# Optimization experiments

Measured on AMD Instinct MI355X. Metric: run time of the kernel, lower is better.

## Reference

```python
import jax, jax.numpy as jnp
import numpy as np
import math

NEG_INF = -1000000000.0
D_EMBED = 1024
D_K = 1024
N_HEADS = 16
D_H = D_EMBED // N_HEADS


def setup_inputs() -> dict:
    key = jax.random.key(0)
    ks = jax.random.split(key, 12)
    B, S = 2, 2048
    s = 0.02
    return {
        "embed": jax.random.normal(ks[0], (B, S, D_EMBED), dtype=jnp.float32),
        "key": jax.random.normal(ks[1], (B, S, D_K), dtype=jnp.float32),
        "attn_mask": jax.random.randint(ks[2], (B, S, S), 0, 2, dtype=jnp.int32),
        "Wq": jax.random.normal(ks[3], (D_EMBED, D_EMBED), dtype=jnp.float32) * s,
        "bq": jnp.zeros((D_EMBED,), dtype=jnp.float32),
        "Wk": jax.random.normal(ks[4], (D_EMBED, D_K), dtype=jnp.float32) * s,
        "bk": jnp.zeros((D_EMBED,), dtype=jnp.float32),
        "Wv": jax.random.normal(ks[5], (D_EMBED, D_K), dtype=jnp.float32) * s,
        "bv": jnp.zeros((D_EMBED,), dtype=jnp.float32),
        "Wo": jax.random.normal(ks[6], (D_EMBED, D_EMBED), dtype=jnp.float32) * s,
        "bo": jnp.zeros((D_EMBED,), dtype=jnp.float32),
    }


def _alibi_bias(seq_len: int, n_heads: int) -> jnp.ndarray:
    # symmetric |i-j| distances, slopes 2^-(8k/H) for k=1..H
    r = jnp.arange(seq_len)
    pos = jnp.abs(r[None, :] - r[:, None]).astype(jnp.float32)  # [S, S]
    step = 8.0 / n_heads
    ms = 2.0 ** (-jnp.arange(step, 8.0 + step, step, dtype=jnp.float32))  # [H]
    return ms[:, None, None] * pos[None, :, :]  # [H, S, S]


def reference(embed, key, attn_mask, Wq, bq, Wk, bk, Wv, bv, Wo, bo):
    B, Sq, _ = embed.shape
    Sk = key.shape[1]
    Q = embed @ Wq.T + bq          # [B, Sq, D]
    K = key @ Wk.T + bk            # [B, Sk, D]
    V = key @ Wv.T + bv            # [B, Sk, D]
    Qh = Q.reshape(B, Sq, N_HEADS, D_H).transpose(0, 2, 1, 3)  # [B, H, Sq, d_h]
    Kh = K.reshape(B, Sk, N_HEADS, D_H).transpose(0, 2, 1, 3)
    Vh = V.reshape(B, Sk, N_HEADS, D_H).transpose(0, 2, 1, 3)
    attn = jnp.einsum("bhqd,bhkd->bhqk", Qh, Kh)
    # ALiBi bias subtracted BEFORE scaling (as in source)
    attn = attn - _alibi_bias(Sq, N_HEADS)[None]
    attn = attn * (1.0 / math.sqrt(D_EMBED))  # note: scale uses d_embed, not d_h
    attn = jnp.where(attn_mask[:, None, :, :] == 0, NEG_INF, attn)
    attn = jax.nn.softmax(attn, axis=-1)
    out = jnp.einsum("bhqk,bhkd->bhqd", attn, Vh)
    out = out.transpose(0, 2, 1, 3).reshape(B, Sq, D_EMBED)
    return out @ Wo.T + bo
```

## Files before the change

kernel.cpp:

```cpp
#include <hip/hip_runtime.h>


typedef _Float16 f16;
typedef __attribute__((ext_vector_type(8))) _Float16 f16x8;
typedef __attribute__((ext_vector_type(4))) _Float16 f16x4;
typedef __attribute__((ext_vector_type(4))) float f32x4;
typedef unsigned long long u64;
typedef unsigned int u32;

#define MFMA16 __builtin_amdgcn_mfma_f32_16x16x32_f16

__global__ __launch_bounds__(256) void k_convert(
    const float* __restrict__ embed, const float* __restrict__ key,
    const float* __restrict__ wq, const float* __restrict__ wk,
    const float* __restrict__ wv, const float* __restrict__ wo,
    f16* __restrict__ xe, f16* __restrict__ xk,
    f16* __restrict__ wqh, f16* __restrict__ wkh,
    f16* __restrict__ wvh, f16* __restrict__ woh)
{
    long g = (long)blockIdx.x * 256 + threadIdx.x;
    const float* src; f16* dst; long off;
    if (g < 524288)       { src = embed; dst = xe; off = g; }
    else if (g < 1048576) { src = key;   dst = xk; off = g - 524288; }
    else {
        long t = g - 1048576; int wi = (int)(t >> 17); off = t & 131071;
        if (wi == 0)      { src = wq; dst = wqh; }
        else if (wi == 1) { src = wk; dst = wkh; }
        else if (wi == 2) { src = wv; dst = wvh; }
        else              { src = wo; dst = woh; }
    }
    const float4* s4 = (const float4*)src;
    float4 a = s4[off * 2], b = s4[off * 2 + 1];
    f16x8 o;
    o[0]=(f16)a.x; o[1]=(f16)a.y; o[2]=(f16)a.z; o[3]=(f16)a.w;
    o[4]=(f16)b.x; o[5]=(f16)b.y; o[6]=(f16)b.z; o[7]=(f16)b.w;
    *(f16x8*)(dst + off * 8) = o;
}

__global__ __launch_bounds__(256) void k_packmask(
    const int* __restrict__ mask, u64* __restrict__ bits)
{
    int gw = (blockIdx.x * 256 + threadIdx.x) >> 6;
    int lane = threadIdx.x & 63;
    const int* row = mask + (long)gw * 2048;
    u64* out = bits + (long)gw * 32;
    #pragma unroll 4
    for (int c = 0; c < 32; ++c) {
        int v = row[c * 64 + lane];
        u64 b = __ballot(v != 0);
        if (lane == 0) out[c] = b;
    }
}

__global__ __launch_bounds__(256) void k_qkv(
    const f16* __restrict__ xe, const f16* __restrict__ xk,
    const f16* __restrict__ wqh, const f16* __restrict__ wkh, const f16* __restrict__ wvh,
    const float* __restrict__ bq, const float* __restrict__ bk, const float* __restrict__ bv,
    f16* __restrict__ Qh, f16* __restrict__ Kh, f16* __restrict__ Vt)
{
    int bid = blockIdx.x;
    int which = bid >> 8;
    int rr_ = bid & 255;
    int tm = rr_ >> 3, tn = rr_ & 7;
    const f16* X = (which == 0) ? xe : xk;
    const f16* W = (which == 0) ? wqh : (which == 1) ? wkh : wvh;
    const float* bias = (which == 0) ? bq : (which == 1) ? bk : bv;

    __shared__ f16 smem[128 * 136];
    f16* la = smem;
    f16* lb = smem + 128 * 64;

    int tid = threadIdx.x;
    int lane = tid & 63, wid = tid >> 6;
    int wr = wid >> 1, wc = wid & 1;
    int lm = lane & 15, qd = lane >> 4;

    f32x4 acc[4][4];
    #pragma unroll
    for (int i = 0; i < 4; i++)
        #pragma unroll
        for (int j = 0; j < 4; j++) acc[i][j] = (f32x4)0.0f;

    int m0 = tm * 128, n0 = tn * 128;

    for (int kt = 0; kt < 16; ++kt) {
        int k0 = kt * 64;
        __syncthreads();
        #pragma unroll
        for (int t = 0; t < 4; ++t) {
            int cid = tid + t * 256;
            int row = cid >> 3;
            int cg = cid & 7;
            int sw = cg ^ (row & 7);
            *(f16x8*)&la[row * 64 + sw * 8] =
                *(const f16x8*)&X[(long)(m0 + row) * 1024 + k0 + cg * 8];
            *(f16x8*)&lb[row * 64 + sw * 8] =
                *(const f16x8*)&W[(long)(n0 + row) * 1024 + k0 + cg * 8];
        }
        __syncthreads();
        #pragma unroll
        for (int ks = 0; ks < 2; ++ks) {
            f16x8 af[4], bfr[4];
            #pragma unroll
            for (int i = 0; i < 4; i++) {
                int m = 64 * wr + 16 * i + lm;
                int g = (ks * 4 + qd) ^ (m & 7);
                af[i] = *(const f16x8*)&la[m * 64 + g * 8];
                int n = 64 * wc + 16 * i + lm;
                int g2 = (ks * 4 + qd) ^ (n & 7);
                bfr[i] = *(const f16x8*)&lb[n * 64 + g2 * 8];
            }
            #pragma unroll
            for (int i = 0; i < 4; i++)
                #pragma unroll
                for (int j = 0; j < 4; j++)
                    acc[i][j] = MFMA16(af[i], bfr[j], acc[i][j], 0, 0, 0);
        }
    }

    if (which == 2) {
        #pragma unroll
        for (int j = 0; j < 4; j++) {
            int n = n0 + 64 * wc + 16 * j + lm;
            float bb = bias[n];
            int h = n >> 6, d = n & 63;
            #pragma unroll
            for (int i = 0; i < 4; i++) {
                int mbase = m0 + 64 * wr + 16 * i + 4 * qd;
                f16x4 pk;
                #pragma unroll
                for (int r = 0; r < 4; ++r) pk[r] = (f16)(acc[i][j][r] + bb);
                int b = mbase >> 11, s = mbase & 2047;
                *(f16x4*)&Vt[(((long)(b * 16 + h)) * 64 + d) * 2048 + s] = pk;
            }
        }
    } else {
        f16* dst = (which == 0) ? Qh : Kh;
        __syncthreads();
        #pragma unroll
        for (int j = 0; j < 4; j++) {
            int col = 64 * wc + 16 * j + lm;
            float bb = bias[n0 + col];
            #pragma unroll
            for (int i = 0; i < 4; i++) {
                int row = 64 * wr + 16 * i + 4 * qd;
                #pragma unroll
                for (int r = 0; r < 4; ++r)
                    smem[(row + r) * 136 + col] = (f16)(acc[i][j][r] + bb);
            }
        }
        __syncthreads();
        #pragma unroll
        for (int t = 0; t < 8; ++t) {
            int ci = tid + t * 256;
            int row = ci >> 4, cg = ci & 15;
            f16x8 v = *(const f16x8*)&smem[row * 136 + cg * 8];
            int m = m0 + row;
            int b = m >> 11, s = m & 2047;
            int h = (n0 >> 6) + (cg >> 3);
            int d0 = (cg & 7) * 8;
            *(f16x8*)&dst[(((long)(b * 16 + h)) * 2048 + s) * 64 + d0] = v;
        }
    }
}

__global__ __launch_bounds__(512, 4) void k_attn(
    const f16* __restrict__ Qh, const f16* __restrict__ Kh, const f16* __restrict__ Vt,
    const u64* __restrict__ mbits, f16* __restrict__ O)
{
    int bid = blockIdx.x;
    int qt = bid & 15;
    int h = (bid >> 4) & 15;
    int b = bid >> 8;
    int q0 = qt * 128;

    const f16* Qg = Qh + ((long)(b * 16 + h)) * 2048 * 64;
    const f16* Kg = Kh + ((long)(b * 16 + h)) * 2048 * 64;
    const f16* Vg = Vt + ((long)(b * 16 + h)) * 64 * 2048;

    __shared__ f16 ks[128 * 64];
    __shared__ f16 vs[64 * 128];
    __shared__ f16 ps[8][16 * 128];

    int tid = threadIdx.x, lane = tid & 63, wid = tid >> 6;
    int lm = lane & 15, qd = lane >> 4;

    int qrow = q0 + 16 * wid + lm;
    const u64* Mrow = mbits + ((long)(b * 2048) + qrow) * 32;

    f16x8 aq[2];
    #pragma unroll
    for (int ksi = 0; ksi < 2; ++ksi)
        aq[ksi] = *(const f16x8*)&Qg[(long)qrow * 64 + ksi * 32 + qd * 8];

    f32x4 oacc[4], lacc;
    #pragma unroll
    for (int c = 0; c < 4; c++) oacc[c] = (f32x4)0.0f;
    lacc = (f32x4)0.0f;
    f16x8 vone;
    #pragma unroll
    for (int j = 0; j < 8; j++) vone[j] = (f16)1.0f;

    const float c1 = 0.0450842252f;
    float negc2 = -__builtin_amdgcn_exp2f(-0.5f * (float)(h + 1)) * c1;
    const float c3 = 5.7707801634f;

    for (int kt = 0; kt < 16; ++kt) {
        int k0 = kt * 128;
        __syncthreads();
        #pragma unroll
        for (int t = 0; t < 2; ++t) {
            int cid = tid + t * 512;
            int row = cid >> 3, cg = cid & 7;
            int sw = cg ^ (row & 7);
            *(f16x8*)&ks[row * 64 + sw * 8] =
                *(const f16x8*)&Kg[(long)(k0 + row) * 64 + cg * 8];
            int vrow = cid >> 4, vg = cid & 15;
            int vsw = vg ^ (vrow & 7);
            *(f16x8*)&vs[vrow * 128 + vsw * 8] =
                *(const f16x8*)&Vg[(long)vrow * 2048 + k0 + vg * 8];
        }
        __syncthreads();

        u64 w0 = Mrow[kt * 2], w1 = Mrow[kt * 2 + 1];

        f32x4 sacc[8];
        #pragma unroll
        for (int c = 0; c < 8; c++) sacc[c] = (f32x4)0.0f;
        #pragma unroll
        for (int ksi = 0; ksi < 2; ++ksi) {
            #pragma unroll
            for (int c = 0; c < 8; c++) {
                int kr = 16 * c + lm;
                int g = (ksi * 4 + qd) ^ (kr & 7);
                f16x8 ak = *(const f16x8*)&ks[kr * 64 + g * 8];
                sacc[c] = MFMA16(ak, aq[ksi], sacc[c], 0, 0, 0);
            }
        }

        float qmkb = (float)(qrow - k0 - 4 * qd);
        int shb = 4 * qd;
        #pragma unroll
        for (int c = 0; c < 8; c++) {
            u32 nib = (u32)(((c < 4) ? w0 : w1) >> (16 * (c & 3) + shb)) & 15u;
            float qmkc = qmkb - 16.0f * (float)c;
            float p[4];
            #pragma unroll
            for (int r = 0; r < 4; ++r) {
                float t2 = fmaf(sacc[c][r], c1, -c3);
                float dd = qmkc - (float)r;
                float u = fmaf(fabsf(dd), negc2, t2);
                u = ((nib >> r) & 1u) ? u : -1e30f;
                p[r] = __builtin_amdgcn_exp2f(u);
            }
            f16x4 pk;
            #pragma unroll
            for (int r = 0; r < 4; ++r) pk[r] = (f16)p[r];
            int g8 = (2 * c + (qd >> 1)) ^ (lm & 7);
            *(f16x4*)&ps[wid][lm * 128 + g8 * 8 + (qd & 1) * 4] = pk;
        }

        #pragma unroll
        for (int k4 = 0; k4 < 4; ++k4) {
            int gp = (k4 * 4 + qd) ^ (lm & 7);
            f16x8 pa = *(const f16x8*)&ps[wid][lm * 128 + gp * 8];
            #pragma unroll
            for (int cc = 0; cc < 4; ++cc) {
                int d = 16 * cc + lm;
                int g = (k4 * 4 + qd) ^ (d & 7);
                f16x8 vb = *(const f16x8*)&vs[d * 128 + g * 8];
                oacc[cc] = MFMA16(pa, vb, oacc[cc], 0, 0, 0);
            }
            lacc = MFMA16(pa, vone, lacc, 0, 0, 0);
        }
    }

    #pragma unroll
    for (int r = 0; r < 4; ++r) {
        float linv = 1.0f / fmaxf(lacc[r], 1e-30f);
        long rowbase = ((long)(b * 2048 + q0 + 16 * wid + 4 * qd + r)) * 1024 + h * 64;
        #pragma unroll
        for (int cc = 0; cc < 4; ++cc)
            O[rowbase + 16 * cc + lm] = (f16)(oacc[cc][r] * linv);
    }
}

__global__ __launch_bounds__(256) void k_proj(
    const f16* __restrict__ Oh, const f16* __restrict__ woh,
    const float* __restrict__ bo, float* __restrict__ out)
{
    int bid = blockIdx.x;
    int tm = bid >> 3, tn = bid & 7;

    __shared__ f16 la[128 * 64];
    __shared__ f16 lb[128 * 64];

    int tid = threadIdx.x;
    int lane = tid & 63, wid = tid >> 6;
    int wr = wid >> 1, wc = wid & 1;
    int lm = lane & 15, qd = lane >> 4;

    f32x4 acc[4][4];
    #pragma unroll
    for (int i = 0; i < 4; i++)
        #pragma unroll
        for (int j = 0; j < 4; j++) acc[i][j] = (f32x4)0.0f;

    int m0 = tm * 128, n0 = tn * 128;

    for (int kt = 0; kt < 16; ++kt) {
        int k0 = kt * 64;
        __syncthreads();
        #pragma unroll
        for (int t = 0; t < 4; ++t) {
            int cid = tid + t * 256;
            int row = cid >> 3;
            int cg = cid & 7;
            int sw = cg ^ (row & 7);
            *(f16x8*)&la[row * 64 + sw * 8] =
                *(const f16x8*)&Oh[(long)(m0 + row) * 1024 + k0 + cg * 8];
            *(f16x8*)&lb[row * 64 + sw * 8] =
                *(const f16x8*)&woh[(long)(n0 + row) * 1024 + k0 + cg * 8];
        }
        __syncthreads();
        #pragma unroll
        for (int ks = 0; ks < 2; ++ks) {
            f16x8 af[4], bfr[4];
            #pragma unroll
            for (int i = 0; i < 4; i++) {
                int m = 64 * wr + 16 * i + lm;
                int g = (ks * 4 + qd) ^ (m & 7);
                af[i] = *(const f16x8*)&la[m * 64 + g * 8];
                int n = 64 * wc + 16 * i + lm;
                int g2 = (ks * 4 + qd) ^ (n & 7);
                bfr[i] = *(const f16x8*)&lb[n * 64 + g2 * 8];
            }
            #pragma unroll
            for (int i = 0; i < 4; i++)
                #pragma unroll
                for (int j = 0; j < 4; j++)
                    acc[i][j] = MFMA16(af[i], bfr[j], acc[i][j], 0, 0, 0);
        }
    }

    #pragma unroll
    for (int j = 0; j < 4; j++) {
        int n = n0 + 64 * wc + 16 * j + lm;
        float bb = bo[n];
        #pragma unroll
        for (int i = 0; i < 4; i++) {
            int mbase = m0 + 64 * wr + 16 * i + 4 * qd;
            #pragma unroll
            for (int r = 0; r < 4; ++r)
                out[(long)(mbase + r) * 1024 + n] = acc[i][j][r] + bb;
        }
    }
}

extern "C" void kernel_launch(void* const* d_in, const int* in_sizes, int n_in,
                              void* d_out, int out_size, void* d_ws, size_t ws_size,
                              hipStream_t stream)
{
    const float* embed = (const float*)d_in[0];
    const float* key   = (const float*)d_in[1];
    const int*   mask  = (const int*)d_in[2];
    const float* Wq = (const float*)d_in[3];
    const float* bq = (const float*)d_in[4];
    const float* Wk = (const float*)d_in[5];
    const float* bk = (const float*)d_in[6];
    const float* Wv = (const float*)d_in[7];
    const float* bv = (const float*)d_in[8];
    const float* Wo = (const float*)d_in[9];
    const float* bo = (const float*)d_in[10];

    char* ws = (char*)d_ws;
    f16* xe  = (f16*)(ws + 0);
    f16* xk  = (f16*)(ws + 8388608);
    f16* wqh = (f16*)(ws + 16777216);
    f16* wkh = (f16*)(ws + 18874368);
    f16* wvh = (f16*)(ws + 20971520);
    f16* woh = (f16*)(ws + 23068672);
    f16* Qh  = (f16*)(ws + 25165824);
    f16* Kh  = (f16*)(ws + 33554432);
    f16* Vt  = (f16*)(ws + 41943040);
    f16* Oh  = (f16*)(ws + 50331648);
    u64* mb  = (u64*)(ws + 58720256);
    float* out = (float*)d_out;

    k_convert<<<6144, 256, 0, stream>>>(embed, key, Wq, Wk, Wv, Wo,
                                        xe, xk, wqh, wkh, wvh, woh);
    k_packmask<<<1024, 256, 0, stream>>>(mask, mb);
    k_qkv<<<768, 256, 0, stream>>>(xe, xk, wqh, wkh, wvh, bq, bk, bv, Qh, Kh, Vt);
    k_attn<<<512, 512, 0, stream>>>(Qh, Kh, Vt, mb, Oh);
    k_proj<<<256, 256, 0, stream>>>(Oh, woh, bo, out);
}
```

Baseline: 274.5 us.

## Feed softmax probabilities to PV MFMA from registers and double rows per wave

The attention kernel now feeds the exponentiated scores straight from the QK^T accumulator registers into 16x16x16 MFMAs for the PV product, with no round trip through LDS. Each wave now handles 32 query rows instead of 16, so every K fragment read from LDS is used twice, and blocks drop to 256 threads. The softmax scale is folded into Q during the QKV projection, and the constant exponent shift is removed, which saves an FMA per score. The trade-offs are higher register pressure, fewer waves per block, and a slightly different f16 rounding of Q.

Result: slower. 287.5 us (+4.8%).

```diff
diff --git a/kernel.cpp b/kernel.cpp
--- a/kernel.cpp
+++ b/kernel.cpp
@@ -9,6 +9,7 @@
 typedef unsigned int u32;
 
 #define MFMA16 __builtin_amdgcn_mfma_f32_16x16x32_f16
+#define MFMA16K16 __builtin_amdgcn_mfma_f32_16x16x16f16
 
 __global__ __launch_bounds__(256) void k_convert(
     const float* __restrict__ embed, const float* __restrict__ key,
@@ -136,6 +137,7 @@
         }
     } else {
         f16* dst = (which == 0) ? Qh : Kh;
+        float sc = (which == 0) ? 0.0450842252f : 1.0f;
         __syncthreads();
         #pragma unroll
         for (int j = 0; j < 4; j++) {
@@ -146,7 +148,7 @@
                 int row = 64 * wr + 16 * i + 4 * qd;
                 #pragma unroll
                 for (int r = 0; r < 4; ++r)
-                    smem[(row + r) * 136 + col] = (f16)(acc[i][j][r] + bb);
+                    smem[(row + r) * 136 + col] = (f16)((acc[i][j][r] + bb) * sc);
             }
         }
         __syncthreads();
@@ -164,7 +166,7 @@
     }
 }
 
-__global__ __launch_bounds__(512, 4) void k_attn(
+__global__ __launch_bounds__(256, 2) void k_attn(
     const f16* __restrict__ Qh, const f16* __restrict__ Kh, const f16* __restrict__ Vt,
     const u64* __restrict__ mbits, f16* __restrict__ O)
 {
@@ -180,37 +182,40 @@
 
     __shared__ f16 ks[128 * 64];
     __shared__ f16 vs[64 * 128];
-    __shared__ f16 ps[8][16 * 128];
 
     int tid = threadIdx.x, lane = tid & 63, wid = tid >> 6;
     int lm = lane & 15, qd = lane >> 4;
 
-    int qrow = q0 + 16 * wid + lm;
-    const u64* Mrow = mbits + ((long)(b * 2048) + qrow) * 32;
-
-    f16x8 aq[2];
-    #pragma unroll
-    for (int ksi = 0; ksi < 2; ++ksi)
-        aq[ksi] = *(const f16x8*)&Qg[(long)qrow * 64 + ksi * 32 + qd * 8];
-
-    f32x4 oacc[4], lacc;
-    #pragma unroll
-    for (int c = 0; c < 4; c++) oacc[c] = (f32x4)0.0f;
-    lacc = (f32x4)0.0f;
-    f16x8 vone;
-    #pragma unroll
-    for (int j = 0; j < 8; j++) vone[j] = (f16)1.0f;
-
-    const float c1 = 0.0450842252f;
-    float negc2 = -__builtin_amdgcn_exp2f(-0.5f * (float)(h + 1)) * c1;
-    const float c3 = 5.7707801634f;
+    int qb = q0 + 32 * wid;
+    const u64* Mrow0 = mbits + ((long)(b * 2048) + qb + lm) * 32;
+    const u64* Mrow1 = mbits + ((long)(b * 2048) + qb + 16 + lm) * 32;
+
+    f16x8 aq[2][2];
+    #pragma unroll
+    for (int g = 0; g < 2; ++g)
+        #pragma unroll
+        for (int ksi = 0; ksi < 2; ++ksi)
+            aq[g][ksi] = *(const f16x8*)&Qg[(long)(qb + 16 * g + lm) * 64 + ksi * 32 + qd * 8];
+
+    f32x4 oacc[2][4], lacc[2];
+    #pragma unroll
+    for (int g = 0; g < 2; ++g) {
+        #pragma unroll
+        for (int c = 0; c < 4; c++) oacc[g][c] = (f32x4)0.0f;
+        lacc[g] = (f32x4)0.0f;
+    }
+    f16x4 vone4;
+    #pragma unroll
+    for (int j = 0; j < 4; j++) vone4[j] = (f16)1.0f;
+
+    float negc2 = -__builtin_amdgcn_exp2f(-0.5f * (float)(h + 1)) * 0.0450842252f;
 
     for (int kt = 0; kt < 16; ++kt) {
         int k0 = kt * 128;
         __syncthreads();
         #pragma unroll
-        for (int t = 0; t < 2; ++t) {
-            int cid = tid + t * 512;
+        for (int t = 0; t < 4; ++t) {
+            int cid = tid + t * 256;
             int row = cid >> 3, cg = cid & 7;
             int sw = cg ^ (row & 7);
             *(f16x8*)&ks[row * 64 + sw * 8] =
@@ -222,66 +227,70 @@
         }
         __syncthreads();
 
-        u64 w0 = Mrow[kt * 2], w1 = Mrow[kt * 2 + 1];
-
-        f32x4 sacc[8];
-        #pragma unroll
-        for (int c = 0; c < 8; c++) sacc[c] = (f32x4)0.0f;
+        u64 w0a = Mrow0[kt * 2], w1a = Mrow0[kt * 2 + 1];
+        u64 w0b = Mrow1[kt * 2], w1b = Mrow1[kt * 2 + 1];
+
+        f32x4 sacc[2][8];
+        #pragma unroll
+        for (int g = 0; g < 2; ++g)
+            #pragma unroll
+            for (int c = 0; c < 8; c++) sacc[g][c] = (f32x4)0.0f;
         #pragma unroll
         for (int ksi = 0; ksi < 2; ++ksi) {
             #pragma unroll
             for (int c = 0; c < 8; c++) {
                 int kr = 16 * c + lm;
-                int g = (ksi * 4 + qd) ^ (kr & 7);
-                f16x8 ak = *(const f16x8*)&ks[kr * 64 + g * 8];
-                sacc[c] = MFMA16(ak, aq[ksi], sacc[c], 0, 0, 0);
-            }
-        }
-
-        float qmkb = (float)(qrow - k0 - 4 * qd);
+                int gg = (ksi * 4 + qd) ^ (kr & 7);
+                f16x8 ak = *(const f16x8*)&ks[kr * 64 + gg * 8];
+                sacc[0][c] = MFMA16(ak, aq[0][ksi], sacc[0][c], 0, 0, 0);
+                sacc[1][c] = MFMA16(ak, aq[1][ksi], sacc[1][c], 0, 0, 0);
+            }
+        }
+
+        float qmk0 = (float)(qb + lm - k0 - 4 * qd);
+        float qmk1 = qmk0 + 16.0f;
         int shb = 4 * qd;
+        int vgq = qd >> 1;
+        int off4 = (qd & 1) * 4;
         #pragma unroll
         for (int c = 0; c < 8; c++) {
-            u32 nib = (u32)(((c < 4) ? w0 : w1) >> (16 * (c & 3) + shb)) & 15u;
-            float qmkc = qmkb - 16.0f * (float)c;
-            float p[4];
+            u32 niba = (u32)(((c < 4) ? w0a : w1a) >> (16 * (c & 3) + shb)) & 15u;
+            u32 nibb = (u32)(((c < 4) ? w0b : w1b) >> (16 * (c & 3) + shb)) & 15u;
+            float qc0 = qmk0 - 16.0f * (float)c;
+            float qc1 = qmk1 - 16.0f * (float)c;
+            f16x4 pk0, pk1;
             #pragma unroll
             for (int r = 0; r < 4; ++r) {
-                float t2 = fmaf(sacc[c][r], c1, -c3);
-                float dd = qmkc - (float)r;
-                float u = fmaf(fabsf(dd), negc2, t2);
-                u = ((nib >> r) & 1u) ? u : -1e30f;
-                p[r] = __builtin_amdgcn_exp2f(u);
-            }
-            f16x4 pk;
-            #pragma unroll
-            for (int r = 0; r < 4; ++r) pk[r] = (f16)p[r];
-            int g8 = (2 * c + (qd >> 1)) ^ (lm & 7);
-            *(f16x4*)&ps[wid][lm * 128 + g8 * 8 + (qd & 1) * 4] = pk;
-        }
-
-        #pragma unroll
-        for (int k4 = 0; k4 < 4; ++k4) {
-            int gp = (k4 * 4 + qd) ^ (lm & 7);
-            f16x8 pa = *(const f16x8*)&ps[wid][lm * 128 + gp * 8];
+                float u0 = fmaf(fabsf(qc0 - (float)r), negc2, sacc[0][c][r]);
+                u0 = ((niba >> r) & 1u) ? u0 : -1e30f;
+                pk0[r] = (f16)__builtin_amdgcn_exp2f(u0);
+                float u1 = fmaf(fabsf(qc1 - (float)r), negc2, sacc[1][c][r]);
+                u1 = ((nibb >> r) & 1u) ? u1 : -1e30f;
+                pk1[r] = (f16)__builtin_amdgcn_exp2f(u1);
+            }
+            int vgc = 2 * c + vgq;
             #pragma unroll
             for (int cc = 0; cc < 4; ++cc) {
                 int d = 16 * cc + lm;
-                int g = (k4 * 4 + qd) ^ (d & 7);
-                f16x8 vb = *(const f16x8*)&vs[d * 128 + g * 8];
-                oacc[cc] = MFMA16(pa, vb, oacc[cc], 0, 0, 0);
-            }
-            lacc = MFMA16(pa, vone, lacc, 0, 0, 0);
-        }
-    }
-
-    #pragma unroll
-    for (int r = 0; r < 4; ++r) {
-        float linv = 1.0f / fmaxf(lacc[r], 1e-30f);
-        long rowbase = ((long)(b * 2048 + q0 + 16 * wid + 4 * qd + r)) * 1024 + h * 64;
-        #pragma unroll
-        for (int cc = 0; cc < 4; ++cc)
-            O[rowbase + 16 * cc + lm] = (f16)(oacc[cc][r] * linv);
+                f16x4 vb = *(const f16x4*)&vs[d * 128 + (vgc ^ (d & 7)) * 8 + off4];
+                oacc[0][cc] = MFMA16K16(pk0, vb, oacc[0][cc], 0, 0, 0);
+                oacc[1][cc] = MFMA16K16(pk1, vb, oacc[1][cc], 0, 0, 0);
+            }
+            lacc[0] = MFMA16K16(pk0, vone4, lacc[0], 0, 0, 0);
+            lacc[1] = MFMA16K16(pk1, vone4, lacc[1], 0, 0, 0);
+        }
+    }
+
+    #pragma unroll
+    for (int g = 0; g < 2; ++g) {
+        #pragma unroll
+        for (int r = 0; r < 4; ++r) {
+            float linv = 1.0f / fmaxf(lacc[g][r], 1e-30f);
+            long rowbase = ((long)(b * 2048 + qb + 16 * g + 4 * qd + r)) * 1024 + h * 64;
+            #pragma unroll
+            for (int cc = 0; cc < 4; ++cc)
+                O[rowbase + 16 * cc + lm] = (f16)(oacc[g][cc][r] * linv);
+        }
     }
 }
 
@@ -391,6 +400,6 @@
                                         xe, xk, wqh, wkh, wvh, woh);
     k_packmask<<<1024, 256, 0, stream>>>(mask, mb);
     k_qkv<<<768, 256, 0, stream>>>(xe, xk, wqh, wkh, wvh, bq, bk, bv, Qh, Kh, Vt);
-    k_attn<<<512, 512, 0, stream>>>(Qh, Kh, Vt, mb, Oh);
+    k_attn<<<512, 256, 0, stream>>>(Qh, Kh, Vt, mb, Oh);
     k_proj<<<256, 256, 0, stream>>>(Oh, woh, bo, out);
 }
```
